# Optimization experiments

Hardware: AMD Instinct MI355X
Metric: run time of the kernel (lower is better)

## Reference

```python
import jax, jax.numpy as jnp
import numpy as np

# Dimensions
B_, L_, D_ = 2, 1024, 1024
EXPAND, N_STATE, K_CONV = 2, 16, 4
D_INNER = D_ * EXPAND          # 2048
DT_RANK = (D_ + 15) // 16      # 64 (mamba default: ceil(d_model/16))


def setup_inputs() -> dict:
    key = jax.random.key(0)
    ks = jax.random.split(key, 10)
    sc = 0.02
    x = jax.random.normal(ks[0], (B_, L_, D_), jnp.float32)
    ln_w = jnp.ones((D_,), jnp.float32)
    ln_b = jnp.zeros((D_,), jnp.float32)
    W_in = jax.random.normal(ks[1], (2 * D_INNER, D_), jnp.float32) * sc
    W_conv = jax.random.normal(ks[2], (D_INNER, K_CONV), jnp.float32) * 0.2
    b_conv = jnp.zeros((D_INNER,), jnp.float32)
    W_xproj = jax.random.normal(ks[3], (DT_RANK + 2 * N_STATE, D_INNER), jnp.float32) * sc
    W_dt = jax.random.normal(ks[4], (D_INNER, DT_RANK), jnp.float32) * (DT_RANK ** -0.5)
    # dt bias: inverse softplus of dt ~ U[1e-3, 1e-1] (mamba init)
    dt = jnp.exp(jax.random.uniform(ks[5], (D_INNER,), jnp.float32)
                 * (np.log(0.1) - np.log(0.001)) + np.log(0.001))
    b_dt = dt + jnp.log(-jnp.expm1(-dt))
    # A_log init: log(1..N) per channel (S4D-real init)
    A_log = jnp.log(jnp.broadcast_to(jnp.arange(1, N_STATE + 1, dtype=jnp.float32),
                                     (D_INNER, N_STATE)))
    D_skip = jnp.ones((D_INNER,), jnp.float32)
    W_out = jax.random.normal(ks[6], (D_, D_INNER), jnp.float32) * sc
    return {"x": x, "ln_w": ln_w, "ln_b": ln_b, "W_in": W_in, "W_conv": W_conv,
            "b_conv": b_conv, "W_xproj": W_xproj, "W_dt": W_dt, "b_dt": b_dt,
            "A_log": A_log, "D_skip": D_skip, "W_out": W_out}


def _layernorm(x, w, b, eps=1e-5):
    mu = jnp.mean(x, axis=-1, keepdims=True)
    var = jnp.mean(jnp.square(x - mu), axis=-1, keepdims=True)
    return (x - mu) * jax.lax.rsqrt(var + eps) * w + b


def reference(x, ln_w, ln_b, W_in, W_conv, b_conv, W_xproj, W_dt, b_dt,
              A_log, D_skip, W_out):
    B, L, D = x.shape
    residual = x
    xn = _layernorm(x, ln_w, ln_b)

    # in_proj -> (x_ssm, z), each (B, L, d_inner)
    xz = jnp.einsum('bld,ed->ble', xn, W_in)
    xs, z = jnp.split(xz, 2, axis=-1)

    # causal depthwise conv1d along L + SiLU
    xp = jnp.pad(xs, ((0, 0), (K_CONV - 1, 0), (0, 0)))
    xc = b_conv + sum(xp[:, k:k + L, :] * W_conv[:, k] for k in range(K_CONV))
    xc = jax.nn.silu(xc)

    # input-dependent dt, B, C
    dbl = jnp.einsum('ble,re->blr', xc, W_xproj)
    dt_low = dbl[..., :DT_RANK]
    B_ssm = dbl[..., DT_RANK:DT_RANK + N_STATE]        # (B, L, N)
    C_ssm = dbl[..., DT_RANK + N_STATE:]               # (B, L, N)
    delta = jax.nn.softplus(jnp.einsum('blr,er->ble', dt_low, W_dt) + b_dt)  # (B, L, d_inner)

    A = -jnp.exp(A_log)                                # (d_inner, N)
    dA = jnp.exp(delta[..., None] * A)                 # (B, L, d_inner, N)
    dBx = delta[..., None] * B_ssm[:, :, None, :] * xc[..., None]  # (B, L, d_inner, N)

    def step(h, inp):
        dA_t, dBx_t, C_t = inp
        h = dA_t * h + dBx_t                           # (B, d_inner, N)
        y_t = jnp.einsum('bdn,bn->bd', h, C_t)
        return h, y_t

    h0 = jnp.zeros((B, D_INNER, N_STATE), x.dtype)
    _, ys = jax.lax.scan(step, h0,
                         (dA.transpose(1, 0, 2, 3), dBx.transpose(1, 0, 2, 3),
                          C_ssm.transpose(1, 0, 2)))
    y = ys.transpose(1, 0, 2) + D_skip * xc            # (B, L, d_inner)
    y = y * jax.nn.silu(z)
    out = jnp.einsum('ble,de->bld', y, W_out)
    # dropout is identity in eval mode
    return out + residual
```

## Files before the change

### kernel.cpp

```cpp
#include <hip/hip_runtime.h>
#include <math.h>

#define B_ 2
#define L_ 1024
#define D_ 1024
#define D_INNER 2048
#define DT_RANK 64
#define N_STATE 16
#define NC 64
#define LC 16

typedef __attribute__((ext_vector_type(8))) short bf16x8;
typedef __attribute__((ext_vector_type(4))) float f32x4;

__device__ __forceinline__ unsigned short f2bf(float f) {
  unsigned int u = __float_as_uint(f);
  u += 0x7fffu + ((u >> 16) & 1u);
  return (unsigned short)(u >> 16);
}
__device__ __forceinline__ float bf2f(unsigned short s) {
  return __uint_as_float((unsigned int)s << 16);
}
__device__ __forceinline__ float softplus_f(float v) {
  return (v > 20.0f) ? v : log1pf(__expf(v));
}

#define N4_WIN  1048576
#define N4_WOUT  524288
#define N4_WDT    32768
#define N4_WXP    65536
#define N4_ZERO   49152
#define N4_CPY   524288
#define PREP_F4 (N4_WIN + N4_WOUT + N4_WDT + N4_WXP + N4_ZERO + N4_CPY)
#define PREP_BLOCKS (2048 + (PREP_F4 + 255) / 256)

__global__ __launch_bounds__(256) void prep_kernel(const float* __restrict__ x,
                                                   const float* __restrict__ w,
                                                   const float* __restrict__ b,
                                                   unsigned short* __restrict__ xn_b,
                                                   const float* __restrict__ W_in,
                                                   const float* __restrict__ W_out,
                                                   const float* __restrict__ W_dt,
                                                   const float* __restrict__ W_xp,
                                                   unsigned short* __restrict__ Win_b,
                                                   unsigned short* __restrict__ Wout_b,
                                                   unsigned short* __restrict__ Wdt_b,
                                                   unsigned short* __restrict__ Wxp_b,
                                                   float* __restrict__ dblb,
                                                   float* __restrict__ outb) {
  if (blockIdx.x < 2048) {
    int row = blockIdx.x;
    int tid = threadIdx.x;
    const float* xr = x + (size_t)row * D_;
    float4 v = ((const float4*)xr)[tid];
    float s  = v.x + v.y + v.z + v.w;
    float s2 = v.x*v.x + v.y*v.y + v.z*v.z + v.w*v.w;
    #pragma unroll
    for (int off = 32; off > 0; off >>= 1) {
      s  += __shfl_down(s, off);
      s2 += __shfl_down(s2, off);
    }
    __shared__ float ss[4], ss2[4];
    int wid = tid >> 6, lane = tid & 63;
    if (lane == 0) { ss[wid] = s; ss2[wid] = s2; }
    __syncthreads();
    if (tid == 0) {
      float a  = ss[0] + ss[1] + ss[2] + ss[3];
      float a2 = ss2[0] + ss2[1] + ss2[2] + ss2[3];
      ss[0]  = a  * (1.0f / D_);
      ss2[0] = a2 * (1.0f / D_);
    }
    __syncthreads();
    float mu = ss[0];
    float var = ss2[0] - mu * mu;
    float rstd = rsqrtf(var + 1e-5f);
    float4 wv = ((const float4*)w)[tid];
    float4 bv = ((const float4*)b)[tid];
    ushort4 o;
    o.x = f2bf((v.x - mu) * rstd * wv.x + bv.x);
    o.y = f2bf((v.y - mu) * rstd * wv.y + bv.y);
    o.z = f2bf((v.z - mu) * rstd * wv.z + bv.z);
    o.w = f2bf((v.w - mu) * rstd * wv.w + bv.w);
    ((ushort4*)(xn_b + (size_t)row * D_))[tid] = o;
    return;
  }
  int i = (blockIdx.x - 2048) * 256 + threadIdx.x;
  if (i < N4_WIN) {
    float4 v = ((const float4*)W_in)[i];
    ushort4 o; o.x = f2bf(v.x); o.y = f2bf(v.y); o.z = f2bf(v.z); o.w = f2bf(v.w);
    ((ushort4*)Win_b)[i] = o;
    return;
  }
  i -= N4_WIN;
  if (i < N4_WOUT) {
    float4 v = ((const float4*)W_out)[i];
    ushort4 o; o.x = f2bf(v.x); o.y = f2bf(v.y); o.z = f2bf(v.z); o.w = f2bf(v.w);
    ((ushort4*)Wout_b)[i] = o;
    return;
  }
  i -= N4_WOUT;
  if (i < N4_WDT) {
    float4 v = ((const float4*)W_dt)[i];
    ushort4 o; o.x = f2bf(v.x); o.y = f2bf(v.y); o.z = f2bf(v.z); o.w = f2bf(v.w);
    ((ushort4*)Wdt_b)[i] = o;
    return;
  }
  i -= N4_WDT;
  if (i < N4_WXP) {
    int row = (i * 4) >> 11;
    ushort4 o = make_ushort4(0, 0, 0, 0);
    if (row < 96) {
      float4 v = ((const float4*)W_xp)[i];
      o.x = f2bf(v.x); o.y = f2bf(v.y); o.z = f2bf(v.z); o.w = f2bf(v.w);
    }
    ((ushort4*)Wxp_b)[i] = o;
    return;
  }
  i -= N4_WXP;
  if (i < N4_ZERO) {
    ((float4*)dblb)[i] = make_float4(0.f, 0.f, 0.f, 0.f);
    return;
  }
  i -= N4_ZERO;
  if (i < N4_CPY) {
    ((float4*)outb)[i] = ((const float4*)x)[i];
  }
}

template<int EPI, int BMT>
__global__ __launch_bounds__(256) void gemm_mfma(const unsigned short* __restrict__ A, int lda,
                                                 const unsigned short* __restrict__ B, int ldb,
                                                 float* __restrict__ Cf,
                                                 unsigned short* __restrict__ Cb,
                                                 int ldc, int Nguard, int K,
                                                 const float* __restrict__ ep0,
                                                 const float* __restrict__ Af32 = nullptr) {
  __shared__ unsigned short As[BMT * 64];
  __shared__ unsigned short Bs[128 * 64];
  const int tid = threadIdx.x;
  const int lane = tid & 63;
  const int w = tid >> 6;
  const int wr = w >> 1, wc = w & 1;
  int flat = blockIdx.y * gridDim.x + blockIdx.x;
  int nwg = gridDim.x * gridDim.y;
  int q8 = nwg >> 3;
  int swz = (flat & 7) * q8 + (flat >> 3);
  const int bm = (swz / gridDim.x) * BMT;
  const int bn = (swz % gridDim.x) * 128;
  const int l16 = lane & 15;
  constexpr int MW = BMT / 32;

  int kbeg = 0, kend = K;
  if (EPI == 6 || EPI == 7) {
    int ks = K / gridDim.z;
    kbeg = blockIdx.z * ks;
    kend = kbeg + ks;
  }

  f32x4 acc[MW][4];
  #pragma unroll
  for (int m = 0; m < MW; ++m)
    #pragma unroll
    for (int n = 0; n < 4; ++n) acc[m][n] = (f32x4){0.f, 0.f, 0.f, 0.f};

  for (int k0 = kbeg; k0 < kend; k0 += 64) {
    if constexpr (EPI == 5) {
      #pragma unroll
      for (int i = 0; i < BMT / 32; ++i) {
        int p = (i * 256 + tid) * 16;
        int r = p >> 7;
        int s = (p >> 4) & 7;
        int cb = ((s ^ (r & 7)) << 3);
        const float* ga = Af32 + (size_t)(bm + r) * lda + cb;
        float4 v0 = *(const float4*)ga;
        float4 v1 = *(const float4*)(ga + 4);
        ushort4 u0 = make_ushort4(f2bf(v0.x), f2bf(v0.y), f2bf(v0.z), f2bf(v0.w));
        ushort4 u1 = make_ushort4(f2bf(v1.x), f2bf(v1.y), f2bf(v1.z), f2bf(v1.w));
        *(ushort4*)(As + (p >> 1)) = u0;
        *(ushort4*)(As + (p >> 1) + 4) = u1;
      }
    } else if constexpr (EPI == 6) {
      #pragma unroll
      for (int i = 0; i < BMT / 32; ++i) {
        int p = (i * 256 + tid) * 16;
        int r = p >> 7;
        int s = (p >> 4) & 7;
        int cb = ((s ^ (r & 7)) << 3);
        int tg = bm + r;
        int tt = tg & (L_ - 1);
        int e  = k0 + cb;
        const unsigned short* bp = A + (size_t)tg * lda + e;
        bf16x8 x0 = *(const bf16x8*)bp;
        bf16x8 xm1 = (bf16x8)(short)0, xm2 = (bf16x8)(short)0, xm3 = (bf16x8)(short)0;
        if (tt >= 1) xm1 = *(const bf16x8*)(bp - lda);
        if (tt >= 2) xm2 = *(const bf16x8*)(bp - 2 * lda);
        if (tt >= 3) xm3 = *(const bf16x8*)(bp - 3 * lda);
        unsigned short res[8];
        #pragma unroll
        for (int j = 0; j < 8; ++j) {
          float4 wv = ((const float4*)Af32)[e + j];
          float a = ep0[e + j];
          a = fmaf(bf2f((unsigned short)xm3[j]), wv.x, a);
          a = fmaf(bf2f((unsigned short)xm2[j]), wv.y, a);
          a = fmaf(bf2f((unsigned short)xm1[j]), wv.z, a);
          a = fmaf(bf2f((unsigned short)x0[j]),  wv.w, a);
          float sv = a / (1.0f + __expf(-a));
          res[j] = f2bf(sv);
        }
        ushort4 u0 = make_ushort4(res[0], res[1], res[2], res[3]);
        ushort4 u1 = make_ushort4(res[4], res[5], res[6], res[7]);
        *(ushort4*)(As + (p >> 1)) = u0;
        *(ushort4*)(As + (p >> 1) + 4) = u1;
        unsigned short* xo = Cb + (size_t)tg * D_INNER + e;
        *(ushort4*)xo = u0;
        *(ushort4*)(xo + 4) = u1;
      }
    } else {
      #pragma unroll
      for (int i = 0; i < BMT / 32; ++i) {
        int p = (i * 256 + tid) * 16;
        int r = p >> 7;
        int s = (p >> 4) & 7;
        int cb = ((s ^ (r & 7)) << 3);
        const unsigned short* ga = A + (size_t)(bm + r) * lda + k0 + cb;
        __builtin_amdgcn_global_load_lds(
            (const __attribute__((address_space(1))) void*)ga,
            (__attribute__((address_space(3))) void*)(As + (p >> 1)), 16, 0, 0);
      }
    }
    #pragma unroll
    for (int i = 0; i < 4; ++i) {
      int p = (i * 256 + tid) * 16;
      int r = p >> 7;
      int s = (p >> 4) & 7;
      int cb = ((s ^ (r & 7)) << 3);
      const unsigned short* gb = B + (size_t)(bn + r) * ldb + k0 + cb;
      __builtin_amdgcn_global_load_lds(
          (const __attribute__((address_space(1))) void*)gb,
          (__attribute__((address_space(3))) void*)(Bs + (p >> 1)), 16, 0, 0);
    }
    __syncthreads();
    #pragma unroll
    for (int ks = 0; ks < 2; ++ks) {
      const int slot = ks * 4 + (lane >> 4);
      bf16x8 af[MW], bfr[4];
      #pragma unroll
      for (int m = 0; m < MW; ++m) {
        int ar = wr * (BMT / 2) + m * 16 + l16;
        af[m] = *(const bf16x8*)(As + ar * 64 + ((slot ^ (ar & 7)) << 3));
      }
      #pragma unroll
      for (int n = 0; n < 4; ++n) {
        int br = wc * 64 + n * 16 + l16;
        bfr[n] = *(const bf16x8*)(Bs + br * 64 + ((slot ^ (br & 7)) << 3));
      }
      #pragma unroll
      for (int m = 0; m < MW; ++m)
        #pragma unroll
        for (int n = 0; n < 4; ++n)
          acc[m][n] = __builtin_amdgcn_mfma_f32_16x16x32_bf16(af[m], bfr[n], acc[m][n], 0, 0, 0);
    }
    __syncthreads();
  }

  const int crow0 = bm + wr * (BMT / 2) + (lane >> 4) * 4;
  const int ccol0 = bn + wc * 64 + l16;
  #pragma unroll
  for (int m = 0; m < MW; ++m) {
    #pragma unroll
    for (int n = 0; n < 4; ++n) {
      int c = ccol0 + n * 16;
      if (c >= Nguard) continue;
      #pragma unroll
      for (int r = 0; r < 4; ++r) {
        int rr = crow0 + m * 16 + r;
        float v = acc[m][n][r];
        if (EPI == 1) {
          Cb[(size_t)rr * ldc + c] = f2bf(v);
        } else if (EPI == 6 || EPI == 7) {
          atomicAdd(&Cf[(size_t)rr * ldc + c], v);
        } else if (EPI == 5) {
          Cb[(size_t)rr * ldc + c] = f2bf(softplus_f(v + ep0[c]));
        } else {
          Cf[(size_t)rr * ldc + c] = v;
        }
      }
    }
  }
}

__global__ __launch_bounds__(256) void scan1_kernel(const unsigned short* __restrict__ delta,
                                                    const unsigned short* __restrict__ xc,
                                                    const float* __restrict__ dbl,
                                                    const float* __restrict__ A_log,
                                                    float* __restrict__ P,
                                                    float* __restrict__ Q) {
  int e = blockIdx.x * 256 + threadIdx.x;
  int b = blockIdx.y, c = blockIdx.z;
  const int t0 = (int)(b * L_ + c * LC);

  __shared__ float sB[LC][N_STATE];
  {
    int step = threadIdx.x >> 4, n = threadIdx.x & 15;
    sB[step][n] = dbl[(size_t)(t0 + step) * 96 + 64 + n];
  }
  __syncthreads();

  float An[N_STATE];
  #pragma unroll
  for (int q = 0; q < 4; ++q) {
    float4 v = *(const float4*)&A_log[(size_t)e * N_STATE + q * 4];
    An[q*4+0] = -__expf(v.x); An[q*4+1] = -__expf(v.y);
    An[q*4+2] = -__expf(v.z); An[q*4+3] = -__expf(v.w);
  }
  float h[N_STATE], p[N_STATE];
  #pragma unroll
  for (int n = 0; n < N_STATE; ++n) { h[n] = 0.f; p[n] = 1.f; }

  const size_t row0 = (size_t)t0 * D_INNER + e;
  float dlt = bf2f(delta[row0]);
  float xcv = bf2f(xc[row0]);

  for (int tt = 0; tt < LC; ++tt) {
    float ndlt = 0.f, nxcv = 0.f;
    if (tt + 1 < LC) {
      ndlt = bf2f(delta[row0 + (size_t)(tt + 1) * D_INNER]);
      nxcv = bf2f(xc[row0 + (size_t)(tt + 1) * D_INNER]);
    }
    float dbx = dlt * xcv;
    #pragma unroll
    for (int n = 0; n < N_STATE; ++n) {
      float da = __expf(dlt * An[n]);
      h[n] = fmaf(da, h[n], dbx * sB[tt][n]);
      p[n] *= da;
    }
    dlt = ndlt; xcv = nxcv;
  }
  size_t o = ((size_t)(c * B_ + b) * N_STATE) * D_INNER + e;
  #pragma unroll
  for (int n = 0; n < N_STATE; ++n) {
    P[o + (size_t)n * D_INNER] = p[n];
    Q[o + (size_t)n * D_INNER] = h[n];
  }
}

__global__ __launch_bounds__(256) void scan2_kernel(const float* __restrict__ P,
                                                    float* __restrict__ Q) {
  int idx = blockIdx.x * 256 + threadIdx.x;
  float H = 0.f;
  #pragma unroll
  for (int c = 0; c < NC; ++c) {
    size_t o = (size_t)c * (B_ * N_STATE * D_INNER) + idx;
    float p = P[o], q = Q[o];
    Q[o] = H;
    H = fmaf(p, H, q);
  }
}

__global__ __launch_bounds__(256) void scan3_kernel(const unsigned short* __restrict__ delta,
                                                    const unsigned short* __restrict__ xc,
                                                    const float* __restrict__ dbl,
                                                    const float* __restrict__ A_log,
                                                    const float* __restrict__ Hinit,
                                                    const unsigned short* __restrict__ xz,
                                                    const float* __restrict__ Dsk,
                                                    unsigned short* __restrict__ y) {
  int e = blockIdx.x * 256 + threadIdx.x;
  int b = blockIdx.y, c = blockIdx.z;
  const int t0 = (int)(b * L_ + c * LC);

  __shared__ float sB[LC][N_STATE];
  __shared__ float sC[LC][N_STATE];
  {
    int step = threadIdx.x >> 4, n = threadIdx.x & 15;
    const float* row = dbl + (size_t)(t0 + step) * 96;
    sB[step][n] = row[64 + n];
    sC[step][n] = row[80 + n];
  }
  __syncthreads();

  float An[N_STATE];
  #pragma unroll
  for (int q = 0; q < 4; ++q) {
    float4 v = *(const float4*)&A_log[(size_t)e * N_STATE + q * 4];
    An[q*4+0] = -__expf(v.x); An[q*4+1] = -__expf(v.y);
    An[q*4+2] = -__expf(v.z); An[q*4+3] = -__expf(v.w);
  }
  float h[N_STATE];
  {
    size_t o = ((size_t)(c * B_ + b) * N_STATE) * D_INNER + e;
    #pragma unroll
    for (int n = 0; n < N_STATE; ++n) h[n] = Hinit[o + (size_t)n * D_INNER];
  }
  float dskip = Dsk[e];
  const size_t row0 = (size_t)t0 * D_INNER + e;
  const size_t zrow0 = (size_t)t0 * 4096 + D_INNER + e;

  float dlt = bf2f(delta[row0]);
  float xcv = bf2f(xc[row0]);
  float zv  = bf2f(xz[zrow0]);

  for (int tt = 0; tt < LC; ++tt) {
    float ndlt = 0.f, nxcv = 0.f, nzv = 0.f;
    if (tt + 1 < LC) {
      ndlt = bf2f(delta[row0 + (size_t)(tt + 1) * D_INNER]);
      nxcv = bf2f(xc[row0 + (size_t)(tt + 1) * D_INNER]);
      nzv  = bf2f(xz[zrow0 + (size_t)(tt + 1) * 4096]);
    }
    float dbx = dlt * xcv;
    float yv = 0.f;
    #pragma unroll
    for (int n = 0; n < N_STATE; ++n) {
      float da = __expf(dlt * An[n]);
      h[n] = fmaf(da, h[n], dbx * sB[tt][n]);
      yv = fmaf(h[n], sC[tt][n], yv);
    }
    float gate = zv / (1.0f + __expf(-zv));
    y[row0 + (size_t)tt * D_INNER] = f2bf((yv + dskip * xcv) * gate);
    dlt = ndlt; xcv = nxcv; zv = nzv;
  }
}

extern "C" void kernel_launch(void* const* d_in, const int* in_sizes, int n_in,
                              void* d_out, int out_size, void* d_ws, size_t ws_size,
                              hipStream_t stream) {
  const float* x       = (const float*)d_in[0];
  const float* ln_w    = (const float*)d_in[1];
  const float* ln_b    = (const float*)d_in[2];
  const float* W_in    = (const float*)d_in[3];
  const float* W_conv  = (const float*)d_in[4];
  const float* b_conv  = (const float*)d_in[5];
  const float* W_xproj = (const float*)d_in[6];
  const float* W_dt    = (const float*)d_in[7];
  const float* b_dt    = (const float*)d_in[8];
  const float* A_log   = (const float*)d_in[9];
  const float* D_skip  = (const float*)d_in[10];
  const float* W_out   = (const float*)d_in[11];
  float* out = (float*)d_out;

  const size_t BL = (size_t)B_ * L_;
  float* dblb = (float*)d_ws;
  float* P    = dblb + 196608;
  float* Q    = P    + 4194304;
  unsigned short* xn_b    = (unsigned short*)(Q + 4194304);
  unsigned short* Win_b   = xn_b    + 2097152;
  unsigned short* xz_b    = Win_b   + 4194304;
  unsigned short* xc_b    = xz_b    + 8388608;
  unsigned short* Wxp_b   = xc_b    + 4194304;
  unsigned short* y_b     = Wxp_b   + 262144;
  unsigned short* Wout_b  = y_b     + 4194304;
  unsigned short* Wdt_b   = Wout_b  + 2097152;
  unsigned short* delta_b = Wdt_b   + 131072;

  prep_kernel<<<PREP_BLOCKS, 256, 0, stream>>>(
      x, ln_w, ln_b, xn_b, W_in, W_out, W_dt, W_xproj,
      Win_b, Wout_b, Wdt_b, Wxp_b, dblb, out);
  gemm_mfma<1, 64><<<dim3(32, 32), 256, 0, stream>>>(
      xn_b, D_, Win_b, D_, nullptr, xz_b, 4096, 4096, D_, nullptr);
  gemm_mfma<6, 128><<<dim3(1, 16, 16), 256, 0, stream>>>(
      xz_b, 4096, Wxp_b, D_INNER, dblb, xc_b, 96, 96, D_INNER, b_conv, W_conv);
  gemm_mfma<5, 128><<<dim3(16, 16), 256, 0, stream>>>(
      nullptr, 96, Wdt_b, DT_RANK, nullptr, delta_b, D_INNER, D_INNER, DT_RANK, b_dt, dblb);
  scan1_kernel<<<dim3(D_INNER / 256, B_, NC), 256, 0, stream>>>(delta_b, xc_b, dblb, A_log, P, Q);
  scan2_kernel<<<(B_ * N_STATE * D_INNER) / 256, 256, 0, stream>>>(P, Q);
  scan3_kernel<<<dim3(D_INNER / 256, B_, NC), 256, 0, stream>>>(delta_b, xc_b, dblb, A_log, Q,
                                                                xz_b, D_skip, y_b);
  gemm_mfma<7, 64><<<dim3(8, 32, 2), 256, 0, stream>>>(
      y_b, D_INNER, Wout_b, D_INNER, out, nullptr, D_, D_, D_INNER, nullptr);
}
```

Measured before the change: 250.5 us.

## Fuse residual add into out_proj epilogue and batch scan2 loads

The out-projection GEMM no longer uses a split-K with atomicAdd into an output buffer pre-filled with the residual copy. It now runs a single-pass GEMM whose epilogue adds x directly, which removes the residual copy from prep and the atomic traffic. The change halves the grid of the out-proj GEMM (256 blocks instead of 512), so each block does twice the K work with less parallelism. Separately, scan2 loads 16 chunks of P and Q ahead of the dependent recurrence to expose memory-level parallelism.

```diff
diff --git a/kernel.cpp b/kernel.cpp
--- a/kernel.cpp
+++ b/kernel.cpp
@@ -30,8 +30,7 @@
 #define N4_WDT    32768
 #define N4_WXP    65536
 #define N4_ZERO   49152
-#define N4_CPY   524288
-#define PREP_F4 (N4_WIN + N4_WOUT + N4_WDT + N4_WXP + N4_ZERO + N4_CPY)
+#define PREP_F4 (N4_WIN + N4_WOUT + N4_WDT + N4_WXP + N4_ZERO)
 #define PREP_BLOCKS (2048 + (PREP_F4 + 255) / 256)
 
 __global__ __launch_bounds__(256) void prep_kernel(const float* __restrict__ x,
@@ -46,8 +45,7 @@
                                                    unsigned short* __restrict__ Wout_b,
                                                    unsigned short* __restrict__ Wdt_b,
                                                    unsigned short* __restrict__ Wxp_b,
-                                                   float* __restrict__ dblb,
-                                                   float* __restrict__ outb) {
+                                                   float* __restrict__ dblb) {
   if (blockIdx.x < 2048) {
     int row = blockIdx.x;
     int tid = threadIdx.x;
@@ -119,11 +117,6 @@
   i -= N4_WXP;
   if (i < N4_ZERO) {
     ((float4*)dblb)[i] = make_float4(0.f, 0.f, 0.f, 0.f);
-    return;
-  }
-  i -= N4_ZERO;
-  if (i < N4_CPY) {
-    ((float4*)outb)[i] = ((const float4*)x)[i];
   }
 }
 
@@ -151,7 +144,7 @@
   constexpr int MW = BMT / 32;
 
   int kbeg = 0, kend = K;
-  if (EPI == 6 || EPI == 7) {
+  if (EPI == 6) {
     int ks = K / gridDim.z;
     kbeg = blockIdx.z * ks;
     kend = kbeg + ks;
@@ -277,7 +270,9 @@
         float v = acc[m][n][r];
         if (EPI == 1) {
           Cb[(size_t)rr * ldc + c] = f2bf(v);
-        } else if (EPI == 6 || EPI == 7) {
+        } else if (EPI == 2) {
+          Cf[(size_t)rr * ldc + c] = v + ep0[(size_t)rr * ldc + c];
+        } else if (EPI == 6) {
           atomicAdd(&Cf[(size_t)rr * ldc + c], v);
         } else if (EPI == 5) {
           Cb[(size_t)rr * ldc + c] = f2bf(softplus_f(v + ep0[c]));
@@ -347,13 +342,23 @@
 __global__ __launch_bounds__(256) void scan2_kernel(const float* __restrict__ P,
                                                     float* __restrict__ Q) {
   int idx = blockIdx.x * 256 + threadIdx.x;
+  const int STRIDE = B_ * N_STATE * D_INNER;
   float H = 0.f;
   #pragma unroll
-  for (int c = 0; c < NC; ++c) {
-    size_t o = (size_t)c * (B_ * N_STATE * D_INNER) + idx;
-    float p = P[o], q = Q[o];
-    Q[o] = H;
-    H = fmaf(p, H, q);
+  for (int g = 0; g < NC / 16; ++g) {
+    float pv[16], qv[16];
+    #pragma unroll
+    for (int j = 0; j < 16; ++j) {
+      size_t o = (size_t)(g * 16 + j) * STRIDE + idx;
+      pv[j] = P[o];
+      qv[j] = Q[o];
+    }
+    #pragma unroll
+    for (int j = 0; j < 16; ++j) {
+      size_t o = (size_t)(g * 16 + j) * STRIDE + idx;
+      Q[o] = H;
+      H = fmaf(pv[j], H, qv[j]);
+    }
   }
 }
 
@@ -454,7 +459,7 @@
 
   prep_kernel<<<PREP_BLOCKS, 256, 0, stream>>>(
       x, ln_w, ln_b, xn_b, W_in, W_out, W_dt, W_xproj,
-      Win_b, Wout_b, Wdt_b, Wxp_b, dblb, out);
+      Win_b, Wout_b, Wdt_b, Wxp_b, dblb);
   gemm_mfma<1, 64><<<dim3(32, 32), 256, 0, stream>>>(
       xn_b, D_, Win_b, D_, nullptr, xz_b, 4096, 4096, D_, nullptr);
   gemm_mfma<6, 128><<<dim3(1, 16, 16), 256, 0, stream>>>(
@@ -465,6 +470,6 @@
   scan2_kernel<<<(B_ * N_STATE * D_INNER) / 256, 256, 0, stream>>>(P, Q);
   scan3_kernel<<<dim3(D_INNER / 256, B_, NC), 256, 0, stream>>>(delta_b, xc_b, dblb, A_log, Q,
                                                                 xz_b, D_skip, y_b);
-  gemm_mfma<7, 64><<<dim3(8, 32, 2), 256, 0, stream>>>(
-      y_b, D_INNER, Wout_b, D_INNER, out, nullptr, D_, D_, D_INNER, nullptr);
-}
+  gemm_mfma<2, 64><<<dim3(8, 32), 256, 0, stream>>>(
+      y_b, D_INNER, Wout_b, D_INNER, out, nullptr, D_, D_, D_INNER, x);
+}
```

After: 377.6 us. 50.7% more time.
